# Kernel optimization log

Hardware: AMD Instinct MI355X
Metric: run time of the kernel (lower is better)

Reference implementation:

```python
import jax, jax.numpy as jnp
import numpy as np

B, S, H, G, DH = 2, 2048, 16, 4, 64
D = H * DH        # 1024
DKV = G * DH      # 256
SCALE = 1.0 / np.sqrt(DH).astype(np.float32)


def apply_rope(x, rope):
    # x: [..., S, DH]; rope: [2, S, DH] (rope[0]=cos, rope[1]=sin)
    xr = x.reshape(*x.shape[:-1], DH // 2, 2)
    x_rot = jnp.stack([-xr[..., 1], xr[..., 0]], axis=-1).reshape(x.shape)
    return x * rope[0] + x_rot * rope[1]


def setup_inputs() -> dict:
    key = jax.random.key(0)
    ks = jax.random.split(key, 5)
    X = jax.random.normal(ks[0], (B, S, D), dtype=jnp.float32)
    Wq = jax.random.normal(ks[1], (D, D), dtype=jnp.float32) / np.sqrt(D).astype(np.float32)
    Wk = jax.random.normal(ks[2], (DKV, D), dtype=jnp.float32) / np.sqrt(D).astype(np.float32)
    Wv = jax.random.normal(ks[3], (DKV, D), dtype=jnp.float32) / np.sqrt(D).astype(np.float32)
    Wo = jax.random.normal(ks[4], (D, D), dtype=jnp.float32) / np.sqrt(D).astype(np.float32)
    # standard RoPE angles, interleaved (pairs (0,1),(2,3),...)
    pos = jnp.arange(S, dtype=jnp.float32)
    inv_freq = 1.0 / (10000.0 ** (jnp.arange(0, DH, 2, dtype=jnp.float32) / DH))
    ang = pos[:, None] * inv_freq[None, :]          # [S, DH/2]
    ang = jnp.repeat(ang, 2, axis=-1)               # [S, DH]
    rope = jnp.stack([jnp.cos(ang), jnp.sin(ang)])  # [2, S, DH]
    causal = jnp.tril(jnp.ones((S, S), dtype=bool))
    return {"X": X, "Wq": Wq, "Wk": Wk, "Wv": Wv, "Wo": Wo, "rope": rope, "causal": causal}


def reference(X, Wq, Wk, Wv, Wo, rope, causal):
    # QKV projections (torch Linear: y = x @ W.T)
    Q = (X @ Wq.T).reshape(B, S, H, DH).transpose(0, 2, 1, 3)   # [B,H,S,DH]
    K = (X @ Wk.T).reshape(B, S, G, DH).transpose(0, 2, 1, 3)   # [B,G,S,DH]
    V = (X @ Wv.T).reshape(B, S, G, DH).transpose(0, 2, 1, 3)   # [B,G,S,DH]
    Q = apply_rope(Q, rope)
    K = apply_rope(K, rope)
    # GQA: repeat KV heads (repeat_interleave semantics)
    K = jnp.repeat(K, H // G, axis=1)                            # [B,H,S,DH]
    V = jnp.repeat(V, H // G, axis=1)
    scores = SCALE * jnp.einsum('bhqd,bhkd->bhqk', Q, K)         # [B,H,S,S]
    scores = jnp.where(causal, scores, -jnp.inf)
    A = jax.nn.softmax(scores, axis=-1)
    Y = jnp.einsum('bhqk,bhkd->bhqd', A, V)                      # [B,H,S,DH]
    Y = Y.transpose(0, 2, 1, 3).reshape(B, S, D)
    return Y @ Wo.T
```

## Files before the change

kernel.cpp:

```cpp
#include <hip/hip_runtime.h>
#include <hip/hip_bf16.h>

#define B_   2
#define S_   2048
#define H_   16
#define G_   4
#define DH_  64
#define D_   1024
#define DKV_ 256
#define SCALE_ 0.125f
#define LDQK_ 1280

using short8  = __attribute__((ext_vector_type(8))) short;
using floatx4 = __attribute__((ext_vector_type(4))) float;
typedef unsigned short ushort_t;

__device__ __forceinline__ ushort_t f2bf(float f) {
    union { float f; unsigned u; } v; v.f = f;
    unsigned r = v.u + 0x7fffu + ((v.u >> 16) & 1u);
    return (ushort_t)(r >> 16);
}
__device__ __forceinline__ float bf2f(ushort_t u) {
    union { unsigned u; float f; } v; v.u = ((unsigned)u) << 16;
    return v.f;
}
__device__ __forceinline__ unsigned cvt_pk_bf16(float lo, float hi) {
    unsigned r;
    asm("v_cvt_pk_bf16_f32 %0, %1, %2" : "=v"(r) : "v"(lo), "v"(hi));
    return r;
}

__device__ __forceinline__ void gload16(const ushort_t* g, ushort_t* l) {
    __builtin_amdgcn_global_load_lds(
        (const __attribute__((address_space(1))) void*)g,
        (__attribute__((address_space(3))) void*)l, 16, 0, 0);
}

__global__ void pack_all(const float* __restrict__ X,  const float* __restrict__ Wq,
                         const float* __restrict__ Wk, const float* __restrict__ Wv,
                         const float* __restrict__ Wo, ushort_t* __restrict__ dst) {
    const int X4  = B_ * S_ * D_ / 4;
    const int QW4 = D_ * D_ / 4;
    const int KW4 = DKV_ * D_ / 4;
    int i = blockIdx.x * blockDim.x + threadIdx.x;
    const float* src; int off;
    if (i < X4)                        { src = X;  off = i; }
    else if (i < X4 + QW4)             { src = Wq; off = i - X4; }
    else if (i < X4 + QW4 + KW4)       { src = Wk; off = i - X4 - QW4; }
    else if (i < X4 + QW4 + 2 * KW4)   { src = Wv; off = i - X4 - QW4 - KW4; }
    else                               { src = Wo; off = i - X4 - QW4 - 2 * KW4; }
    float4 v = reinterpret_cast<const float4*>(src)[off];
    ushort4 o;
    o.x = f2bf(v.x); o.y = f2bf(v.y); o.z = f2bf(v.z); o.w = f2bf(v.w);
    reinterpret_cast<ushort4*>(dst)[i] = o;
}

__global__ __launch_bounds__(256)
void gemm_all(int mode,
              const ushort_t* __restrict__ Xb,  const ushort_t* __restrict__ Wqkb,
              const ushort_t* __restrict__ Wvb, const ushort_t* __restrict__ Wob,
              ushort_t* __restrict__ QKb, ushort_t* __restrict__ Vtb,
              const ushort_t* __restrict__ Yb, float* __restrict__ Cout,
              const float* __restrict__ rope, float qscale)
{
    __shared__ __align__(16) ushort_t Asm[2][128 * 64];
    __shared__ __align__(16) ushort_t Bsm[2][64 * 64];

    const ushort_t *Aorig, *Borig;
    ushort_t* Cb = nullptr; float* Cf = nullptr;
    int m0, n0, ldc, epi;
    if (mode == 1) {
        m0 = blockIdx.x * 128; n0 = blockIdx.y * 64;
        Aorig = Yb; Borig = Wob; Cf = Cout; ldc = D_; epi = 1;
    } else {
        const int bx = blockIdx.x;
        if (bx < 640) {
            m0 = (bx / 20) * 128; n0 = (bx % 20) * 64;
            Aorig = Xb; Borig = Wqkb; Cb = QKb; ldc = LDQK_; epi = 2;
        } else {
            const int idx = bx - 640, b = idx >> 6, rem = idx & 63;
            m0 = (rem >> 5) * 128; n0 = (rem & 31) * 64;
            Aorig = Wvb; Borig = Xb + (long)b * S_ * D_;
            Cb = Vtb + (long)b * DKV_ * S_; ldc = S_; epi = 0;
        }
    }

    const int tid = threadIdx.x, l = tid & 63, w = tid >> 6;
    const int wr = (w >> 1) * 64, wc = (w & 1) * 32;
    const int lr = l & 15, lkb = l >> 4;

    const int srow = w * 8 + (l >> 3);
    const int scol = ((l & 7) ^ ((l >> 3) & 7)) * 8;
    const ushort_t* Ast = Aorig + (long)(m0 + srow) * D_ + scol;
    const ushort_t* Bst = Borig + (long)(n0 + srow) * D_ + scol;

#define GSTAGE(buf, kt)                                                    \
    {                                                                      \
        _Pragma("unroll")                                                  \
        for (int rr = 0; rr < 4; ++rr)                                     \
            gload16(Ast + (long)rr * 32 * D_ + (kt), &Asm[buf][w * 512 + rr * 2048]); \
        _Pragma("unroll")                                                  \
        for (int c = 0; c < 2; ++c)                                        \
            gload16(Bst + (long)c * 32 * D_ + (kt), &Bsm[buf][w * 512 + c * 2048]);   \
    }

    floatx4 acc[4][2] = {};
    const int xr = (lr & 7) << 4;
    GSTAGE(0, 0);
    for (int i = 0; i < 16; ++i) {
        const int cur = i & 1;
        if (i < 15) {
            GSTAGE(cur ^ 1, (i + 1) * 64);
            asm volatile("s_waitcnt vmcnt(6)" ::: "memory");
        } else {
            asm volatile("s_waitcnt vmcnt(0)" ::: "memory");
        }
        __builtin_amdgcn_s_barrier();

#pragma unroll
        for (int ks = 0; ks < 2; ++ks) {
            short8 a[4], bb[2];
#pragma unroll
            for (int ii = 0; ii < 4; ++ii) {
                const int row = wr + ii * 16 + lr;
                a[ii] = *(const short8*)&Asm[cur][(row * 128 + ((ks * 64 + lkb * 16) ^ xr)) >> 1];
            }
#pragma unroll
            for (int j = 0; j < 2; ++j) {
                const int row = wc + j * 16 + lr;
                bb[j] = *(const short8*)&Bsm[cur][(row * 128 + ((ks * 64 + lkb * 16) ^ xr)) >> 1];
            }
            __builtin_amdgcn_s_setprio(1);
#pragma unroll
            for (int ii = 0; ii < 4; ++ii)
#pragma unroll
                for (int j = 0; j < 2; ++j)
                    acc[ii][j] = __builtin_amdgcn_mfma_f32_16x16x32_bf16(a[ii], bb[j], acc[ii][j], 0, 0, 0);
            __builtin_amdgcn_s_setprio(0);
        }
        __builtin_amdgcn_s_barrier();
    }
#undef GSTAGE

    const int rrow = lkb * 4;
#pragma unroll
    for (int i = 0; i < 4; ++i) {
#pragma unroll
        for (int j = 0; j < 2; ++j) {
#pragma unroll
            for (int r = 0; r < 4; ++r) {
                const int row = m0 + wr + i * 16 + rrow + r;
                const int col = n0 + wc + j * 16 + lr;
                if (epi == 1) {
                    Cf[(long)row * ldc + col] = acc[i][j][r];
                } else if (epi == 0) {
                    Cb[(long)row * ldc + col] = f2bf(acc[i][j][r]);
                } else {
                    const float v  = acc[i][j][r];
                    const float pv = __shfl_xor(v, 1);
                    const int   s  = row & (S_ - 1);
                    const int   d  = col & (DH_ - 1);
                    const float cc = rope[s * DH_ + d];
                    const float sn = rope[S_ * DH_ + s * DH_ + d];
                    float res = (lr & 1) ? (v * cc + pv * sn) : (v * cc - pv * sn);
                    res *= (col < D_) ? qscale : 1.0f;
                    Cb[(long)row * ldc + col] = f2bf(res);
                }
            }
        }
    }
}

__global__ __launch_bounds__(256)
void attn_kernel(const ushort_t* __restrict__ QK, const ushort_t* __restrict__ Vt,
                 ushort_t* __restrict__ Y0, ushort_t* __restrict__ Y1,
                 float* __restrict__ L0, float* __restrict__ L1)
{
    __shared__ __align__(16) ushort_t Kt [2][64 * 64];
    __shared__ __align__(16) ushort_t Vts[2][64 * 64];

    const int tid = threadIdx.x;
    const int l   = tid & 63;
    const int w   = tid >> 6;
    const int lr  = l & 15, lkb = l >> 4, lk = lkb * 8;
    const int bx = blockIdx.x, h = blockIdx.y, b = blockIdx.z;
    const int g   = h >> 2;

    const int sr  = l >> 3;
    const int sce = ((l & 7) ^ sr) * 8;
    const ushort_t* Ksrc = QK + (long)b * S_ * LDQK_ + D_ + g * DH_ + sce;
    const ushort_t* Vsrc = Vt + (long)(b * G_ + g) * DH_ * S_ + sce;

    const int rl0 = w * 8 + sr, rl1 = 32 + w * 8 + sr;
    const int kr0 = (rl0 & 0x23) | ((rl0 & 0x0C) << 1) | ((rl0 & 0x10) >> 2);
    const int kr1 = (rl1 & 0x23) | ((rl1 & 0x0C) << 1) | ((rl1 & 0x10) >> 2);

    short8 vones;
#pragma unroll
    for (int j = 0; j < 8; ++j) vones[j] = (short)0x3F80;

    for (int seg = 0; seg < 2; ++seg) {
        const int qt   = seg == 0 ? (S_ / 64 - 1 - bx) : bx;
        const int half = seg == 0 ? 1 : 0;
        const int split = (qt + 2) / 2;
        const int t0 = half ? split : 0;
        const int t1 = half ? qt + 1 : split;
        const int qrow0 = qt * 64 + w * 16;

        const ushort_t* Qp = QK + ((long)b * S_ + qrow0 + lr) * LDQK_ + h * DH_ + lk;
        const short8 bq0 = *(const short8*)(Qp);
        const short8 bq1 = *(const short8*)(Qp + 32);

        floatx4 o[4] = {};
        floatx4 osum = {};

        if (t1 > t0) {
            const ushort_t* kp0 = Ksrc + (long)(t0 * 64 + kr0) * LDQK_;
            const ushort_t* kp1 = Ksrc + (long)(t0 * 64 + kr1) * LDQK_;
            const ushort_t* vp0 = Vsrc + (long)rl0 * S_ + t0 * 64;
            const ushort_t* vp1 = Vsrc + (long)rl1 * S_ + t0 * 64;

#define STAGE(buf)                                            \
    {                                                         \
        gload16(kp0, &Kt[buf][w * 512]);                      \
        gload16(vp0, &Vts[buf][w * 512]);                     \
        gload16(kp1, &Kt[buf][2048 + w * 512]);               \
        gload16(vp1, &Vts[buf][2048 + w * 512]);              \
        kp0 += 64 * LDQK_; kp1 += 64 * LDQK_;                 \
        vp0 += 64;         vp1 += 64;                         \
    }

            STAGE(0);
            asm volatile("s_waitcnt vmcnt(0)" ::: "memory");
            __builtin_amdgcn_s_barrier();

            for (int t = t0; t < t1; ++t) {
                const int cur = (t - t0) & 1;
                if (t + 1 < t1) STAGE(cur ^ 1);

                floatx4 sacc[4] = {};
                __builtin_amdgcn_s_setprio(1);
#pragma unroll
                for (int cf = 0; cf < 4; ++cf) {
                    const int row = cf * 16 + lr;
                    const int xr  = (row & 7) << 4;
                    const short8 ak0 = *(const short8*)&Kt[cur][(row * 128 + ((lkb * 16) ^ xr)) >> 1];
                    const short8 ak1 = *(const short8*)&Kt[cur][(row * 128 + ((64 + lkb * 16) ^ xr)) >> 1];
                    sacc[cf] = __builtin_amdgcn_mfma_f32_16x16x32_bf16(ak0, bq0, sacc[cf], 0, 0, 0);
                    sacc[cf] = __builtin_amdgcn_mfma_f32_16x16x32_bf16(ak1, bq1, sacc[cf], 0, 0, 0);
                }
                __builtin_amdgcn_s_setprio(0);

                if (t == qt) {
                    const int qg = qrow0 + lr;
#pragma unroll
                    for (int cf = 0; cf < 4; ++cf) {
                        const int kvb0 = t * 64 + 32 * (cf >> 1) + 8 * lkb + 4 * (cf & 1);
#pragma unroll
                        for (int r = 0; r < 4; ++r)
                            if (kvb0 + r > qg) sacc[cf][r] = -3e38f;
                    }
                }

#pragma unroll
                for (int cf = 0; cf < 4; ++cf)
#pragma unroll
                    for (int r = 0; r < 4; ++r)
                        sacc[cf][r] = exp2f(sacc[cf][r]);

#pragma unroll
                for (int ks = 0; ks < 2; ++ks) {
                    union { unsigned u[4]; short8 s; } pa;
#pragma unroll
                    for (int j = 0; j < 4; ++j) {
                        const int cf = 2 * ks + (j >> 1);
                        const int e  = (j & 1) * 2;
                        pa.u[j] = cvt_pk_bf16(sacc[cf][e], sacc[cf][e + 1]);
                    }
                    __builtin_amdgcn_s_setprio(1);
#pragma unroll
                    for (int df = 0; df < 4; ++df) {
                        const int vrow = df * 16 + lr;
                        const int xr   = (vrow & 7) << 4;
                        const short8 bv = *(const short8*)&Vts[cur][(vrow * 128 + ((ks * 64 + lkb * 16) ^ xr)) >> 1];
                        o[df] = __builtin_amdgcn_mfma_f32_16x16x32_bf16(pa.s, bv, o[df], 0, 0, 0);
                    }
                    osum = __builtin_amdgcn_mfma_f32_16x16x32_bf16(pa.s, vones, osum, 0, 0, 0);
                    __builtin_amdgcn_s_setprio(0);
                }

                asm volatile("s_waitcnt vmcnt(0)" ::: "memory");
                __builtin_amdgcn_s_barrier();
            }
#undef STAGE
        }

        ushort_t* Yp = half ? Y1 : Y0;
        float*    Lp = half ? L1 : L0;
#pragma unroll
        for (int r = 0; r < 4; ++r) {
            const int row = qrow0 + lkb * 4 + r;
#pragma unroll
            for (int df = 0; df < 4; ++df)
                Yp[((long)b * S_ + row) * D_ + h * DH_ + df * 16 + lr] = f2bf(o[df][r]);
            if (lr == 0)
                Lp[((long)b * S_ + row) * H_ + h] = osum[r];
        }
    }
}

__global__ void combine_kernel(ushort_t* __restrict__ Y0, const ushort_t* __restrict__ Y1,
                               const float* __restrict__ L0, const float* __restrict__ L1) {
    const int i  = blockIdx.x * blockDim.x + threadIdx.x;
    const int row = i >> 7;
    const int h   = (i & 127) >> 3;
    const float inv = 1.f / (L0[row * H_ + h] + L1[row * H_ + h]);
    const short8 y0 = ((const short8*)Y0)[i];
    const short8 y1 = ((const short8*)Y1)[i];
    union { unsigned u[4]; short8 s; } o;
#pragma unroll
    for (int j = 0; j < 4; ++j) {
        const float a = (bf2f((ushort_t)y0[2 * j])     + bf2f((ushort_t)y1[2 * j]))     * inv;
        const float c = (bf2f((ushort_t)y0[2 * j + 1]) + bf2f((ushort_t)y1[2 * j + 1])) * inv;
        o.u[j] = cvt_pk_bf16(a, c);
    }
    ((short8*)Y0)[i] = o.s;
}

extern "C" void kernel_launch(void* const* d_in, const int* in_sizes, int n_in,
                              void* d_out, int out_size, void* d_ws, size_t ws_size,
                              hipStream_t stream) {
    const float* X    = (const float*)d_in[0];
    const float* Wq   = (const float*)d_in[1];
    const float* Wk   = (const float*)d_in[2];
    const float* Wv   = (const float*)d_in[3];
    const float* Wo   = (const float*)d_in[4];
    const float* rope = (const float*)d_in[5];
    float* out = (float*)d_out;

    char* ws = (char*)d_ws;
    size_t o = 0;
    ushort_t* Xb   = (ushort_t*)(ws + o); o += (size_t)B_ * S_ * D_ * 2;
    ushort_t* Wqkb = (ushort_t*)(ws + o); o += (size_t)LDQK_ * D_ * 2;
    ushort_t* Wvb  = (ushort_t*)(ws + o); o += (size_t)DKV_ * D_ * 2;
    ushort_t* Wob  = (ushort_t*)(ws + o); o += (size_t)D_ * D_ * 2;
    ushort_t* QKb  = (ushort_t*)(ws + o); o += (size_t)B_ * S_ * LDQK_ * 2;
    ushort_t* Vtb  = (ushort_t*)(ws + o); o += (size_t)B_ * G_ * DH_ * S_ * 2;
    ushort_t* Y1b  = (ushort_t*)(ws + o); o += (size_t)B_ * S_ * D_ * 2;
    float*    L0   = (float*)(ws + o);    o += (size_t)B_ * S_ * H_ * 4;
    float*    L1   = (float*)(ws + o);    o += (size_t)B_ * S_ * H_ * 4;
    ushort_t* Y0   = Xb;

    {
        int n4 = (B_ * S_ * D_ + 2 * D_ * D_ + 2 * DKV_ * D_) / 4;
        pack_all<<<(n4 + 255) / 256, 256, 0, stream>>>(X, Wq, Wk, Wv, Wo, Xb);
    }

    const float SC2 = SCALE_ * 1.44269504f;
    gemm_all<<<dim3(768, 1, 1), 256, 0, stream>>>(
        0, Xb, Wqkb, Wvb, Wob, QKb, Vtb, nullptr, nullptr, rope, SC2);

    attn_kernel<<<dim3(32, H_, B_), 256, 0, stream>>>(QKb, Vtb, Y0, Y1b, L0, L1);

    {
        int nthr = B_ * S_ * D_ / 8;
        combine_kernel<<<nthr / 256, 256, 0, stream>>>(Y0, Y1b, L0, L1);
    }

    gemm_all<<<dim3(32, 16, 1), 256, 0, stream>>>(
        1, Xb, Wqkb, Wvb, Wob, QKb, Vtb, Y0, out, nullptr, 0.f);
}
```

Measured before the change: 101.4 us.

## Use 128-row query tiles with 8 waves sharing each K/V stage in attention

The attention kernel now launches 512 threads per block covering 128 query rows, so each staged 64-row K/V tile is shared by twice as many waves. Each thread issues one K and one V load per stage instead of two. The causal split changes from halving each tile's KV range to splitting at the tile boundary: segment 0 covers KV tiles qt+1..2qt+1 and segment 1 covers 0..qt. This halves the grid and cuts K/V global and LDS traffic per query, at the cost of fewer blocks, heavier per-block load imbalance, and masking now applied on two diagonal tiles.

```diff
diff --git a/kernel.cpp b/kernel.cpp
--- a/kernel.cpp
+++ b/kernel.cpp
@@ -171,7 +171,7 @@
     }
 }
 
-__global__ __launch_bounds__(256)
+__global__ __launch_bounds__(512)
 void attn_kernel(const ushort_t* __restrict__ QK, const ushort_t* __restrict__ Vt,
                  ushort_t* __restrict__ Y0, ushort_t* __restrict__ Y1,
                  float* __restrict__ L0, float* __restrict__ L1)
@@ -191,21 +191,18 @@
     const ushort_t* Ksrc = QK + (long)b * S_ * LDQK_ + D_ + g * DH_ + sce;
     const ushort_t* Vsrc = Vt + (long)(b * G_ + g) * DH_ * S_ + sce;
 
-    const int rl0 = w * 8 + sr, rl1 = 32 + w * 8 + sr;
-    const int kr0 = (rl0 & 0x23) | ((rl0 & 0x0C) << 1) | ((rl0 & 0x10) >> 2);
-    const int kr1 = (rl1 & 0x23) | ((rl1 & 0x0C) << 1) | ((rl1 & 0x10) >> 2);
+    const int rl = w * 8 + sr;
+    const int kr = (rl & 0x23) | ((rl & 0x0C) << 1) | ((rl & 0x10) >> 2);
 
     short8 vones;
 #pragma unroll
     for (int j = 0; j < 8; ++j) vones[j] = (short)0x3F80;
 
     for (int seg = 0; seg < 2; ++seg) {
-        const int qt   = seg == 0 ? (S_ / 64 - 1 - bx) : bx;
-        const int half = seg == 0 ? 1 : 0;
-        const int split = (qt + 2) / 2;
-        const int t0 = half ? split : 0;
-        const int t1 = half ? qt + 1 : split;
-        const int qrow0 = qt * 64 + w * 16;
+        const int qt = seg == 0 ? (S_ / 128 - 1 - bx) : bx;
+        const int t0 = seg == 0 ? qt + 1 : 0;
+        const int t1 = seg == 0 ? 2 * qt + 2 : qt + 1;
+        const int qrow0 = qt * 128 + w * 16;
 
         const ushort_t* Qp = QK + ((long)b * S_ + qrow0 + lr) * LDQK_ + h * DH_ + lk;
         const short8 bq0 = *(const short8*)(Qp);
@@ -214,89 +211,83 @@
         floatx4 o[4] = {};
         floatx4 osum = {};
 
-        if (t1 > t0) {
-            const ushort_t* kp0 = Ksrc + (long)(t0 * 64 + kr0) * LDQK_;
-            const ushort_t* kp1 = Ksrc + (long)(t0 * 64 + kr1) * LDQK_;
-            const ushort_t* vp0 = Vsrc + (long)rl0 * S_ + t0 * 64;
-            const ushort_t* vp1 = Vsrc + (long)rl1 * S_ + t0 * 64;
+        const ushort_t* kp = Ksrc + (long)(t0 * 64 + kr) * LDQK_;
+        const ushort_t* vp = Vsrc + (long)rl * S_ + t0 * 64;
 
 #define STAGE(buf)                                            \
     {                                                         \
-        gload16(kp0, &Kt[buf][w * 512]);                      \
-        gload16(vp0, &Vts[buf][w * 512]);                     \
-        gload16(kp1, &Kt[buf][2048 + w * 512]);               \
-        gload16(vp1, &Vts[buf][2048 + w * 512]);              \
-        kp0 += 64 * LDQK_; kp1 += 64 * LDQK_;                 \
-        vp0 += 64;         vp1 += 64;                         \
-    }
-
-            STAGE(0);
+        gload16(kp, &Kt[buf][w * 512]);                       \
+        gload16(vp, &Vts[buf][w * 512]);                      \
+        kp += 64 * LDQK_;                                     \
+        vp += 64;                                             \
+    }
+
+        STAGE(0);
+        asm volatile("s_waitcnt vmcnt(0)" ::: "memory");
+        __builtin_amdgcn_s_barrier();
+
+        for (int t = t0; t < t1; ++t) {
+            const int cur = (t - t0) & 1;
+            if (t + 1 < t1) STAGE(cur ^ 1);
+
+            floatx4 sacc[4] = {};
+            __builtin_amdgcn_s_setprio(1);
+#pragma unroll
+            for (int cf = 0; cf < 4; ++cf) {
+                const int row = cf * 16 + lr;
+                const int xr  = (row & 7) << 4;
+                const short8 ak0 = *(const short8*)&Kt[cur][(row * 128 + ((lkb * 16) ^ xr)) >> 1];
+                const short8 ak1 = *(const short8*)&Kt[cur][(row * 128 + ((64 + lkb * 16) ^ xr)) >> 1];
+                sacc[cf] = __builtin_amdgcn_mfma_f32_16x16x32_bf16(ak0, bq0, sacc[cf], 0, 0, 0);
+                sacc[cf] = __builtin_amdgcn_mfma_f32_16x16x32_bf16(ak1, bq1, sacc[cf], 0, 0, 0);
+            }
+            __builtin_amdgcn_s_setprio(0);
+
+            if (t >= 2 * qt) {
+                const int qg = qrow0 + lr;
+#pragma unroll
+                for (int cf = 0; cf < 4; ++cf) {
+                    const int kvb0 = t * 64 + 32 * (cf >> 1) + 8 * lkb + 4 * (cf & 1);
+#pragma unroll
+                    for (int r = 0; r < 4; ++r)
+                        if (kvb0 + r > qg) sacc[cf][r] = -3e38f;
+                }
+            }
+
+#pragma unroll
+            for (int cf = 0; cf < 4; ++cf)
+#pragma unroll
+                for (int r = 0; r < 4; ++r)
+                    sacc[cf][r] = exp2f(sacc[cf][r]);
+
+#pragma unroll
+            for (int ks = 0; ks < 2; ++ks) {
+                union { unsigned u[4]; short8 s; } pa;
+#pragma unroll
+                for (int j = 0; j < 4; ++j) {
+                    const int cf = 2 * ks + (j >> 1);
+                    const int e  = (j & 1) * 2;
+                    pa.u[j] = cvt_pk_bf16(sacc[cf][e], sacc[cf][e + 1]);
+                }
+                __builtin_amdgcn_s_setprio(1);
+#pragma unroll
+                for (int df = 0; df < 4; ++df) {
+                    const int vrow = df * 16 + lr;
+                    const int xr   = (vrow & 7) << 4;
+                    const short8 bv = *(const short8*)&Vts[cur][(vrow * 128 + ((ks * 64 + lkb * 16) ^ xr)) >> 1];
+                    o[df] = __builtin_amdgcn_mfma_f32_16x16x32_bf16(pa.s, bv, o[df], 0, 0, 0);
+                }
+                osum = __builtin_amdgcn_mfma_f32_16x16x32_bf16(pa.s, vones, osum, 0, 0, 0);
+                __builtin_amdgcn_s_setprio(0);
+            }
+
             asm volatile("s_waitcnt vmcnt(0)" ::: "memory");
             __builtin_amdgcn_s_barrier();
-
-            for (int t = t0; t < t1; ++t) {
-                const int cur = (t - t0) & 1;
-                if (t + 1 < t1) STAGE(cur ^ 1);
-
-                floatx4 sacc[4] = {};
-                __builtin_amdgcn_s_setprio(1);
-#pragma unroll
-                for (int cf = 0; cf < 4; ++cf) {
-                    const int row = cf * 16 + lr;
-                    const int xr  = (row & 7) << 4;
-                    const short8 ak0 = *(const short8*)&Kt[cur][(row * 128 + ((lkb * 16) ^ xr)) >> 1];
-                    const short8 ak1 = *(const short8*)&Kt[cur][(row * 128 + ((64 + lkb * 16) ^ xr)) >> 1];
-                    sacc[cf] = __builtin_amdgcn_mfma_f32_16x16x32_bf16(ak0, bq0, sacc[cf], 0, 0, 0);
-                    sacc[cf] = __builtin_amdgcn_mfma_f32_16x16x32_bf16(ak1, bq1, sacc[cf], 0, 0, 0);
-                }
-                __builtin_amdgcn_s_setprio(0);
-
-                if (t == qt) {
-                    const int qg = qrow0 + lr;
-#pragma unroll
-                    for (int cf = 0; cf < 4; ++cf) {
-                        const int kvb0 = t * 64 + 32 * (cf >> 1) + 8 * lkb + 4 * (cf & 1);
-#pragma unroll
-                        for (int r = 0; r < 4; ++r)
-                            if (kvb0 + r > qg) sacc[cf][r] = -3e38f;
-                    }
-                }
-
-#pragma unroll
-                for (int cf = 0; cf < 4; ++cf)
-#pragma unroll
-                    for (int r = 0; r < 4; ++r)
-                        sacc[cf][r] = exp2f(sacc[cf][r]);
-
-#pragma unroll
-                for (int ks = 0; ks < 2; ++ks) {
-                    union { unsigned u[4]; short8 s; } pa;
-#pragma unroll
-                    for (int j = 0; j < 4; ++j) {
-                        const int cf = 2 * ks + (j >> 1);
-                        const int e  = (j & 1) * 2;
-                        pa.u[j] = cvt_pk_bf16(sacc[cf][e], sacc[cf][e + 1]);
-                    }
-                    __builtin_amdgcn_s_setprio(1);
-#pragma unroll
-                    for (int df = 0; df < 4; ++df) {
-                        const int vrow = df * 16 + lr;
-                        const int xr   = (vrow & 7) << 4;
-                        const short8 bv = *(const short8*)&Vts[cur][(vrow * 128 + ((ks * 64 + lkb * 16) ^ xr)) >> 1];
-                        o[df] = __builtin_amdgcn_mfma_f32_16x16x32_bf16(pa.s, bv, o[df], 0, 0, 0);
-                    }
-                    osum = __builtin_amdgcn_mfma_f32_16x16x32_bf16(pa.s, vones, osum, 0, 0, 0);
-                    __builtin_amdgcn_s_setprio(0);
-                }
-
-                asm volatile("s_waitcnt vmcnt(0)" ::: "memory");
-                __builtin_amdgcn_s_barrier();
-            }
+        }
 #undef STAGE
-        }
-
-        ushort_t* Yp = half ? Y1 : Y0;
-        float*    Lp = half ? L1 : L0;
+
+        ushort_t* Yp = seg == 0 ? Y1 : Y0;
+        float*    Lp = seg == 0 ? L1 : L0;
 #pragma unroll
         for (int r = 0; r < 4; ++r) {
             const int row = qrow0 + lkb * 4 + r;
@@ -360,7 +351,7 @@
     gemm_all<<<dim3(768, 1, 1), 256, 0, stream>>>(
         0, Xb, Wqkb, Wvb, Wob, QKb, Vtb, nullptr, nullptr, rope, SC2);
 
-    attn_kernel<<<dim3(32, H_, B_), 256, 0, stream>>>(QKb, Vtb, Y0, Y1b, L0, L1);
+    attn_kernel<<<dim3(S_ / 128, H_, B_), 512, 0, stream>>>(QKb, Vtb, Y0, Y1b, L0, L1);
 
     {
         int nthr = B_ * S_ * D_ / 8;
```

After: 96.80 us. 1.05x faster.
